# Performance work log

Measured on AMD Instinct MI355X. Metric: run time of the kernel, lower is better.

The kernel has to match this reference:

```python
import jax, jax.numpy as jnp
import numpy as np

B, NX, NR, D, H = 8, 512, 512, 256, 256


def setup_inputs() -> dict:
    key = jax.random.key(0)
    ks = jax.random.split(key, 8)
    s = 1.0 / np.sqrt(D)
    sh = 1.0 / np.sqrt(H)
    return {
        "X": jax.random.normal(ks[0], (B, NX, D), dtype=jnp.float32),
        "ref": jax.random.normal(ks[1], (B, NR, D), dtype=jnp.float32),
        "W_X": jax.random.normal(ks[2], (H, D), dtype=jnp.float32) * s,
        "b_X": jax.random.normal(ks[3], (H,), dtype=jnp.float32) * s,
        "W_ref": jax.random.normal(ks[4], (H, D), dtype=jnp.float32) * s,
        "b_ref": jax.random.normal(ks[5], (H,), dtype=jnp.float32) * s,
        "v_w": jax.random.normal(ks[6], (1, H), dtype=jnp.float32) * sh,
        "v_b": jax.random.normal(ks[7], (1,), dtype=jnp.float32) * sh,
    }


def reference(X, ref, W_X, b_X, W_ref, b_ref, v_w, v_b):
    # linear projections: [B, nX, H], [B, nR, H]
    hX = jnp.einsum('bxd,hd->bxh', X, W_X) + b_X
    hR = jnp.einsum('brd,hd->brh', ref, W_ref) + b_ref
    # additive (Bahdanau) scores: [B, nX, nR]
    t = jnp.tanh(hX[:, :, None, :] + hR[:, None, :, :])
    out = jnp.einsum('bxrh,h->bxr', t, v_w[0]) + v_b[0]
    # softmax over the n_X axis (dim=1 in torch)
    attn = jax.nn.softmax(out, axis=1)
    # weighted sum of X per ref position: [B, nR, D]
    weighted_X = jnp.einsum('bxe,bxr->bre', X, attn)
    return weighted_X
```

## Files before the change

kernel.cpp:

```cpp
#include <hip/hip_runtime.h>
#include <math.h>

#define CB 8
#define CNX 512
#define CNR 512
#define CD 256
#define CH 256

__device__ __forceinline__ float fast_rcp(float x) {
#if __has_builtin(__builtin_amdgcn_rcpf)
  return __builtin_amdgcn_rcpf(x);
#else
  return 1.0f / x;
#endif
}
__device__ __forceinline__ float fast_exp2(float x) {
#if __has_builtin(__builtin_amdgcn_exp2f)
  return __builtin_amdgcn_exp2f(x);
#else
  return exp2f(x);
#endif
}

__global__ __launch_bounds__(256) void proj_fused(
    const float* __restrict__ A0, const float* __restrict__ A1,
    const float* __restrict__ W0, const float* __restrict__ W1,
    const float* __restrict__ bias0, const float* __restrict__ bias1,
    float* __restrict__ E0, float* __restrict__ E1) {
  __shared__ float As[16][68];
  __shared__ float Ws[16][68];
  const int K = CD;
  int z = blockIdx.z;
  const float* A = z ? A1 : A0;
  const float* W = z ? W1 : W0;
  const float* bias = z ? bias1 : bias0;
  float* ET = z ? E1 : E0;
  int m0 = blockIdx.x * 64, n0 = blockIdx.y * 64;
  int tid = threadIdx.x;
  int tx = tid & 15, ty = tid >> 4;
  int lrow = tid >> 2, lc4 = tid & 3;
  int krot = (tid >> 6) << 2;
  float acc[4][4] = {};
  const float* pA = A + (size_t)(m0 + lrow) * K + lc4 * 4;
  const float* pW = W + (size_t)(n0 + lrow) * K + lc4 * 4;
  float4 av = *(const float4*)(pA);
  float4 wv = *(const float4*)(pW);
  for (int kt = 0; kt < K; kt += 16) {
    __syncthreads();
    As[lc4 * 4 + 0][lrow] = av.x;
    As[lc4 * 4 + 1][lrow] = av.y;
    As[lc4 * 4 + 2][lrow] = av.z;
    As[lc4 * 4 + 3][lrow] = av.w;
    Ws[lc4 * 4 + 0][lrow] = wv.x;
    Ws[lc4 * 4 + 1][lrow] = wv.y;
    Ws[lc4 * 4 + 2][lrow] = wv.z;
    Ws[lc4 * 4 + 3][lrow] = wv.w;
    __syncthreads();
    if (kt + 16 < K) {
      av = *(const float4*)(pA + kt + 16);
      wv = *(const float4*)(pW + kt + 16);
    }
#pragma unroll
    for (int k = 0; k < 16; k++) {
      int kk = (k + krot) & 15;
      float4 a4 = *(const float4*)&As[kk][ty * 4];
      float4 w4 = *(const float4*)&Ws[kk][tx * 4];
      float am[4] = {a4.x, a4.y, a4.z, a4.w};
      float wm[4] = {w4.x, w4.y, w4.z, w4.w};
#pragma unroll
      for (int i = 0; i < 4; i++)
#pragma unroll
        for (int j = 0; j < 4; j++)
          acc[i][j] = fmaf(am[i], wm[j], acc[i][j]);
    }
  }
  const float K2L = 2.8853900817779268f;
  float4 bv = *(const float4*)(bias + n0 + tx * 4);
  float bm[4] = {bv.x, bv.y, bv.z, bv.w};
  int b = m0 >> 9;
  int xbase = (m0 & 511) + ty * 4;
#pragma unroll
  for (int j = 0; j < 4; j++) {
    int h = n0 + tx * 4 + j;
    float4 o = {fast_exp2(K2L * (acc[0][j] + bm[j])),
                fast_exp2(K2L * (acc[1][j] + bm[j])),
                fast_exp2(K2L * (acc[2][j] + bm[j])),
                fast_exp2(K2L * (acc[3][j] + bm[j]))};
    *(float4*)(ET + ((size_t)b * CH + h) * CNX + xbase) = o;
  }
}

__global__ __launch_bounds__(512) void scores_kernel(
    const float* __restrict__ exT, const float* __restrict__ erT,
    const float* __restrict__ v_w, float* __restrict__ scT) {
  __shared__ float smem[4 * 2048 + 256];
  int b = blockIdx.z;
  int x0 = blockIdx.x * 64, r0 = blockIdx.y * 64;
  int tid = threadIdx.x;
  int g = tid >> 8;
  int t = tid & 255;
  float* xs = smem + g * 4096;
  float* rs = xs + 2048;
  float* vsh = smem + 8192;
  if (tid < 256) vsh[tid] = v_w[tid];
  int tx = t & 15, ty = t >> 4;
  int sr = t >> 4, sc = (t & 15) * 4;
  int wrot = (tid >> 6) & 7;
  const float* pX = exT + (size_t)b * CH * CNX + x0 + sc;
  const float* pR = erT + (size_t)b * CH * CNR + r0 + sc;
  int hb = g * 32;
  float4 xa0 = *(const float4*)(pX + (size_t)(hb + sr) * CNX);
  float4 xa1 = *(const float4*)(pX + (size_t)(hb + sr + 16) * CNX);
  float4 ra0 = *(const float4*)(pR + (size_t)(hb + sr) * CNR);
  float4 ra1 = *(const float4*)(pR + (size_t)(hb + sr + 16) * CNR);
  float acc[4][4] = {};
  for (int hc = hb; hc < CH; hc += 64) {
    __syncthreads();
    *(float4*)&xs[sr * 64 + sc] = xa0;
    *(float4*)&xs[(sr + 16) * 64 + sc] = xa1;
    *(float4*)&rs[sr * 64 + sc] = ra0;
    *(float4*)&rs[(sr + 16) * 64 + sc] = ra1;
    __syncthreads();
    if (hc + 64 < CH) {
      xa0 = *(const float4*)(pX + (size_t)(hc + 64 + sr) * CNX);
      xa1 = *(const float4*)(pX + (size_t)(hc + 64 + sr + 16) * CNX);
      ra0 = *(const float4*)(pR + (size_t)(hc + 64 + sr) * CNR);
      ra1 = *(const float4*)(pR + (size_t)(hc + 64 + sr + 16) * CNR);
    }
#pragma unroll 2
    for (int hq = 0; hq < 8; hq++) {
      int h0 = ((hq + wrot) & 7) * 4;
      float4 vv = *(const float4*)&vsh[hc + h0];
      float4 xv0 = *(const float4*)&xs[(h0 + 0) * 64 + tx * 4];
      float4 xv1 = *(const float4*)&xs[(h0 + 1) * 64 + tx * 4];
      float4 xv2 = *(const float4*)&xs[(h0 + 2) * 64 + tx * 4];
      float4 xv3 = *(const float4*)&xs[(h0 + 3) * 64 + tx * 4];
      float4 rv0 = *(const float4*)&rs[(h0 + 0) * 64 + ty * 4];
      float4 rv1 = *(const float4*)&rs[(h0 + 1) * 64 + ty * 4];
      float4 rv2 = *(const float4*)&rs[(h0 + 2) * 64 + ty * 4];
      float4 rv3 = *(const float4*)&rs[(h0 + 3) * 64 + ty * 4];
      float xm0[4] = {xv0.x, xv0.y, xv0.z, xv0.w};
      float xm1[4] = {xv1.x, xv1.y, xv1.z, xv1.w};
      float xm2[4] = {xv2.x, xv2.y, xv2.z, xv2.w};
      float xm3[4] = {xv3.x, xv3.y, xv3.z, xv3.w};
      float rm0[4] = {rv0.x, rv0.y, rv0.z, rv0.w};
      float rm1[4] = {rv1.x, rv1.y, rv1.z, rv1.w};
      float rm2[4] = {rv2.x, rv2.y, rv2.z, rv2.w};
      float rm3[4] = {rv3.x, rv3.y, rv3.z, rv3.w};
#pragma unroll
      for (int i = 0; i < 4; i++)
#pragma unroll
        for (int j = 0; j < 4; j++) {
          float a = fmaf(rm0[i], xm0[j], 1.0f);
          float bb = fmaf(rm1[i], xm1[j], 1.0f);
          float c = fmaf(rm2[i], xm2[j], 1.0f);
          float d = fmaf(rm3[i], xm3[j], 1.0f);
          float q12 = a * bb, q34 = c * d;
          float p12 = fmaf(vv.y, a, vv.x * bb);
          float p34 = fmaf(vv.w, c, vv.z * d);
          float num = fmaf(p34, q12, p12 * q34);
          acc[i][j] = fmaf(num, fast_rcp(q12 * q34), acc[i][j]);
        }
    }
  }
  __syncthreads();
  float* mg = smem;
  if (g == 1) {
#pragma unroll
    for (int i = 0; i < 4; i++)
#pragma unroll
      for (int j = 0; j < 4; j++)
        mg[t + 256 * (i * 4 + j)] = acc[i][j];
  }
  __syncthreads();
  if (g == 0) {
    float* pO = scT + ((size_t)b * CNR + r0 + ty * 4) * CNX + x0 + tx * 4;
#pragma unroll
    for (int i = 0; i < 4; i++) {
      float4 o = {-2.0f * (acc[i][0] + mg[t + 256 * (i * 4 + 0)]),
                  -2.0f * (acc[i][1] + mg[t + 256 * (i * 4 + 1)]),
                  -2.0f * (acc[i][2] + mg[t + 256 * (i * 4 + 2)]),
                  -2.0f * (acc[i][3] + mg[t + 256 * (i * 4 + 3)])};
      *(float4*)(pO + (size_t)i * CNX) = o;
    }
  }
}

__global__ __launch_bounds__(512) void wsum_fused(
    const float* __restrict__ scT, const float* __restrict__ X,
    float* __restrict__ out) {
  __shared__ float smem[4 * 2176 + 128];
  const float L2E = 1.4426950408889634f;
  int b = blockIdx.z;
  int r0 = blockIdx.x * 64, d0 = blockIdx.y * 64;
  int tid = threadIdx.x;
  int g = tid >> 8;
  int t = tid & 255;
  float* As = smem + g * 4352;
  float* Bs = As + 2176;
  float* dnn = smem + 8704;
  int tx = t & 15, ty = t >> 4;
  int ar = t >> 2, ak = (t & 3) * 4;
  int br = t >> 4, bc = (t & 15) * 4;
  int krot = ((tid >> 6) & 7) * 4;
  int kb = g * 32;
  const float* pS = scT + ((size_t)b * CNR + r0 + ar) * CNX + ak;
  const float* pB = X + (size_t)b * CNX * CD + d0 + bc;
  float acc[4][4] = {};
  float dsum = 0.0f;
  float4 s0 = *(const float4*)(pS + kb);
  float4 s1 = *(const float4*)(pS + kb + 16);
  float4 b0 = *(const float4*)(pB + (size_t)(kb + br) * CD);
  float4 b1 = *(const float4*)(pB + (size_t)(kb + br + 16) * CD);
  for (int kt = kb; kt < CNX; kt += 64) {
    float4 e0 = {fast_exp2(s0.x * L2E), fast_exp2(s0.y * L2E),
                 fast_exp2(s0.z * L2E), fast_exp2(s0.w * L2E)};
    float4 e1 = {fast_exp2(s1.x * L2E), fast_exp2(s1.y * L2E),
                 fast_exp2(s1.z * L2E), fast_exp2(s1.w * L2E)};
    dsum += ((e0.x + e0.y) + (e0.z + e0.w)) + ((e1.x + e1.y) + (e1.z + e1.w));
    __syncthreads();
    As[(ak + 0) * 68 + ar] = e0.x;
    As[(ak + 1) * 68 + ar] = e0.y;
    As[(ak + 2) * 68 + ar] = e0.z;
    As[(ak + 3) * 68 + ar] = e0.w;
    As[(ak + 16) * 68 + ar] = e1.x;
    As[(ak + 17) * 68 + ar] = e1.y;
    As[(ak + 18) * 68 + ar] = e1.z;
    As[(ak + 19) * 68 + ar] = e1.w;
    *(float4*)&Bs[br * 68 + bc] = b0;
    *(float4*)&Bs[(br + 16) * 68 + bc] = b1;
    __syncthreads();
    if (kt + 64 < CNX) {
      s0 = *(const float4*)(pS + kt + 64);
      s1 = *(const float4*)(pS + kt + 80);
      b0 = *(const float4*)(pB + (size_t)(kt + 64 + br) * CD);
      b1 = *(const float4*)(pB + (size_t)(kt + 64 + br + 16) * CD);
    }
#pragma unroll 8
    for (int k = 0; k < 32; k++) {
      int kk = (k + krot) & 31;
      float4 a4 = *(const float4*)&As[kk * 68 + ty * 4];
      float4 b4 = *(const float4*)&Bs[kk * 68 + tx * 4];
      float am[4] = {a4.x, a4.y, a4.z, a4.w};
      float bm[4] = {b4.x, b4.y, b4.z, b4.w};
#pragma unroll
      for (int i = 0; i < 4; i++)
#pragma unroll
        for (int j = 0; j < 4; j++)
          acc[i][j] = fmaf(am[i], bm[j], acc[i][j]);
    }
  }
  dsum += __shfl_xor(dsum, 1, 64);
  dsum += __shfl_xor(dsum, 2, 64);
  if ((t & 3) == 0) dnn[g * 64 + ar] = dsum;
  __syncthreads();
  float* mg = smem;
  if (g == 1) {
#pragma unroll
    for (int i = 0; i < 4; i++)
#pragma unroll
      for (int j = 0; j < 4; j++)
        mg[t + 256 * (i * 4 + j)] = acc[i][j];
  }
  __syncthreads();
  if (g == 0) {
    float invm[4];
#pragma unroll
    for (int i = 0; i < 4; i++)
      invm[i] = fast_rcp(dnn[ty * 4 + i] + dnn[64 + ty * 4 + i]);
    float* pO = out + ((size_t)b * CNR + r0 + ty * 4) * CD + d0 + tx * 4;
#pragma unroll
    for (int i = 0; i < 4; i++) {
      float4 o = {
          (acc[i][0] + mg[t + 256 * (i * 4 + 0)]) * invm[i],
          (acc[i][1] + mg[t + 256 * (i * 4 + 1)]) * invm[i],
          (acc[i][2] + mg[t + 256 * (i * 4 + 2)]) * invm[i],
          (acc[i][3] + mg[t + 256 * (i * 4 + 3)]) * invm[i]};
      *(float4*)(pO + (size_t)i * CD) = o;
    }
  }
}

extern "C" void kernel_launch(void* const* d_in, const int* in_sizes, int n_in,
                              void* d_out, int out_size, void* d_ws, size_t ws_size,
                              hipStream_t stream) {
  const float* X     = (const float*)d_in[0];
  const float* ref   = (const float*)d_in[1];
  const float* W_X   = (const float*)d_in[2];
  const float* b_X   = (const float*)d_in[3];
  const float* W_ref = (const float*)d_in[4];
  const float* b_ref = (const float*)d_in[5];
  const float* v_w   = (const float*)d_in[6];
  float* out = (float*)d_out;
  float* ws  = (float*)d_ws;

  float* exT = ws;
  float* erT = ws + 1048576;
  float* scT = ws + 2097152;

  proj_fused<<<dim3(64, 4, 2), 256, 0, stream>>>(X, ref, W_X, W_ref, b_X, b_ref, exT, erT);
  scores_kernel<<<dim3(8, 8, 8), 512, 0, stream>>>(exT, erT, v_w, scT);
  wsum_fused<<<dim3(8, 4, 8), 512, 0, stream>>>(scT, X, out);
}
```

Baseline: 152.8 us.

## Use split-bf16 MFMA for the projection GEMM instead of FP32 FMAs

Measured after the change: 146.3 us. -4.3%, faster.

```diff
diff --git a/kernel.cpp b/kernel.cpp
--- a/kernel.cpp
+++ b/kernel.cpp
@@ -6,6 +6,9 @@
 #define CNR 512
 #define CD 256
 #define CH 256
+
+typedef __attribute__((ext_vector_type(8))) short short8;
+typedef __attribute__((ext_vector_type(4))) float f32x4;
 
 __device__ __forceinline__ float fast_rcp(float x) {
 #if __has_builtin(__builtin_amdgcn_rcpf)
@@ -22,13 +25,41 @@
 #endif
 }
 
-__global__ __launch_bounds__(256) void proj_fused(
+__device__ __forceinline__ void cvt_store(unsigned short* dstH,
+                                          unsigned short* dstL,
+                                          float4 v0, float4 v1) {
+  unsigned u0x = __float_as_uint(v0.x), u0y = __float_as_uint(v0.y);
+  unsigned u0z = __float_as_uint(v0.z), u0w = __float_as_uint(v0.w);
+  unsigned u1x = __float_as_uint(v1.x), u1y = __float_as_uint(v1.y);
+  unsigned u1z = __float_as_uint(v1.z), u1w = __float_as_uint(v1.w);
+  uint4 H;
+  H.x = (u0x >> 16) | (u0y & 0xFFFF0000u);
+  H.y = (u0z >> 16) | (u0w & 0xFFFF0000u);
+  H.z = (u1x >> 16) | (u1y & 0xFFFF0000u);
+  H.w = (u1z >> 16) | (u1w & 0xFFFF0000u);
+  float r0x = v0.x - __uint_as_float(u0x & 0xFFFF0000u);
+  float r0y = v0.y - __uint_as_float(u0y & 0xFFFF0000u);
+  float r0z = v0.z - __uint_as_float(u0z & 0xFFFF0000u);
+  float r0w = v0.w - __uint_as_float(u0w & 0xFFFF0000u);
+  float r1x = v1.x - __uint_as_float(u1x & 0xFFFF0000u);
+  float r1y = v1.y - __uint_as_float(u1y & 0xFFFF0000u);
+  float r1z = v1.z - __uint_as_float(u1z & 0xFFFF0000u);
+  float r1w = v1.w - __uint_as_float(u1w & 0xFFFF0000u);
+  uint4 L;
+  L.x = (__float_as_uint(r0x) >> 16) | (__float_as_uint(r0y) & 0xFFFF0000u);
+  L.y = (__float_as_uint(r0z) >> 16) | (__float_as_uint(r0w) & 0xFFFF0000u);
+  L.z = (__float_as_uint(r1x) >> 16) | (__float_as_uint(r1y) & 0xFFFF0000u);
+  L.w = (__float_as_uint(r1z) >> 16) | (__float_as_uint(r1w) & 0xFFFF0000u);
+  *(uint4*)dstH = H;
+  *(uint4*)dstL = L;
+}
+
+__global__ __launch_bounds__(256) void proj_mfma(
     const float* __restrict__ A0, const float* __restrict__ A1,
     const float* __restrict__ W0, const float* __restrict__ W1,
     const float* __restrict__ bias0, const float* __restrict__ bias1,
     float* __restrict__ E0, float* __restrict__ E1) {
-  __shared__ float As[16][68];
-  __shared__ float Ws[16][68];
+  __shared__ unsigned short lds[2][4][64][40];
   const int K = CD;
   int z = blockIdx.z;
   const float* A = z ? A1 : A0;
@@ -37,56 +68,71 @@
   float* ET = z ? E1 : E0;
   int m0 = blockIdx.x * 64, n0 = blockIdx.y * 64;
   int tid = threadIdx.x;
-  int tx = tid & 15, ty = tid >> 4;
-  int lrow = tid >> 2, lc4 = tid & 3;
-  int krot = (tid >> 6) << 2;
-  float acc[4][4] = {};
-  const float* pA = A + (size_t)(m0 + lrow) * K + lc4 * 4;
-  const float* pW = W + (size_t)(n0 + lrow) * K + lc4 * 4;
-  float4 av = *(const float4*)(pA);
-  float4 wv = *(const float4*)(pW);
-  for (int kt = 0; kt < K; kt += 16) {
-    __syncthreads();
-    As[lc4 * 4 + 0][lrow] = av.x;
-    As[lc4 * 4 + 1][lrow] = av.y;
-    As[lc4 * 4 + 2][lrow] = av.z;
-    As[lc4 * 4 + 3][lrow] = av.w;
-    Ws[lc4 * 4 + 0][lrow] = wv.x;
-    Ws[lc4 * 4 + 1][lrow] = wv.y;
-    Ws[lc4 * 4 + 2][lrow] = wv.z;
-    Ws[lc4 * 4 + 3][lrow] = wv.w;
-    __syncthreads();
-    if (kt + 16 < K) {
-      av = *(const float4*)(pA + kt + 16);
-      wv = *(const float4*)(pW + kt + 16);
-    }
-#pragma unroll
-    for (int k = 0; k < 16; k++) {
-      int kk = (k + krot) & 15;
-      float4 a4 = *(const float4*)&As[kk][ty * 4];
-      float4 w4 = *(const float4*)&Ws[kk][tx * 4];
-      float am[4] = {a4.x, a4.y, a4.z, a4.w};
-      float wm[4] = {w4.x, w4.y, w4.z, w4.w};
-#pragma unroll
-      for (int i = 0; i < 4; i++)
-#pragma unroll
-        for (int j = 0; j < 4; j++)
-          acc[i][j] = fmaf(am[i], wm[j], acc[i][j]);
+  int lane = tid & 63, w = tid >> 6;
+  int wm = w >> 1, wn = w & 1;
+  int r = tid >> 2, kq = (tid & 3) * 8;
+  const float* pA = A + (size_t)(m0 + r) * K + kq;
+  const float* pW = W + (size_t)(n0 + r) * K + kq;
+  f32x4 acc[2][2] = {};
+  float4 a0 = *(const float4*)(pA);
+  float4 a1 = *(const float4*)(pA + 4);
+  float4 w0 = *(const float4*)(pW);
+  float4 w1 = *(const float4*)(pW + 4);
+  cvt_store(&lds[0][0][r][kq], &lds[0][1][r][kq], a0, a1);
+  cvt_store(&lds[0][2][r][kq], &lds[0][3][r][kq], w0, w1);
+  for (int s = 0; s < 8; s++) {
+    __syncthreads();
+    if (s < 7) {
+      int kt = (s + 1) * 32;
+      a0 = *(const float4*)(pA + kt);
+      a1 = *(const float4*)(pA + kt + 4);
+      w0 = *(const float4*)(pW + kt);
+      w1 = *(const float4*)(pW + kt + 4);
+    }
+    int cur = s & 1;
+    int arow = wm * 32 + (lane & 15);
+    int brow = wn * 32 + (lane & 15);
+    int koff = (lane >> 4) * 8;
+    short8 ah0 = *(const short8*)&lds[cur][0][arow][koff];
+    short8 ah1 = *(const short8*)&lds[cur][0][arow + 16][koff];
+    short8 al0 = *(const short8*)&lds[cur][1][arow][koff];
+    short8 al1 = *(const short8*)&lds[cur][1][arow + 16][koff];
+    short8 bh0 = *(const short8*)&lds[cur][2][brow][koff];
+    short8 bh1 = *(const short8*)&lds[cur][2][brow + 16][koff];
+    short8 bl0 = *(const short8*)&lds[cur][3][brow][koff];
+    short8 bl1 = *(const short8*)&lds[cur][3][brow + 16][koff];
+    acc[0][0] = __builtin_amdgcn_mfma_f32_16x16x32_bf16(ah0, bh0, acc[0][0], 0, 0, 0);
+    acc[0][1] = __builtin_amdgcn_mfma_f32_16x16x32_bf16(ah0, bh1, acc[0][1], 0, 0, 0);
+    acc[1][0] = __builtin_amdgcn_mfma_f32_16x16x32_bf16(ah1, bh0, acc[1][0], 0, 0, 0);
+    acc[1][1] = __builtin_amdgcn_mfma_f32_16x16x32_bf16(ah1, bh1, acc[1][1], 0, 0, 0);
+    acc[0][0] = __builtin_amdgcn_mfma_f32_16x16x32_bf16(ah0, bl0, acc[0][0], 0, 0, 0);
+    acc[0][1] = __builtin_amdgcn_mfma_f32_16x16x32_bf16(ah0, bl1, acc[0][1], 0, 0, 0);
+    acc[1][0] = __builtin_amdgcn_mfma_f32_16x16x32_bf16(ah1, bl0, acc[1][0], 0, 0, 0);
+    acc[1][1] = __builtin_amdgcn_mfma_f32_16x16x32_bf16(ah1, bl1, acc[1][1], 0, 0, 0);
+    acc[0][0] = __builtin_amdgcn_mfma_f32_16x16x32_bf16(al0, bh0, acc[0][0], 0, 0, 0);
+    acc[0][1] = __builtin_amdgcn_mfma_f32_16x16x32_bf16(al0, bh1, acc[0][1], 0, 0, 0);
+    acc[1][0] = __builtin_amdgcn_mfma_f32_16x16x32_bf16(al1, bh0, acc[1][0], 0, 0, 0);
+    acc[1][1] = __builtin_amdgcn_mfma_f32_16x16x32_bf16(al1, bh1, acc[1][1], 0, 0, 0);
+    if (s < 7) {
+      int nxt = cur ^ 1;
+      cvt_store(&lds[nxt][0][r][kq], &lds[nxt][1][r][kq], a0, a1);
+      cvt_store(&lds[nxt][2][r][kq], &lds[nxt][3][r][kq], w0, w1);
     }
   }
   const float K2L = 2.8853900817779268f;
-  float4 bv = *(const float4*)(bias + n0 + tx * 4);
-  float bm[4] = {bv.x, bv.y, bv.z, bv.w};
   int b = m0 >> 9;
-  int xbase = (m0 & 511) + ty * 4;
-#pragma unroll
-  for (int j = 0; j < 4; j++) {
-    int h = n0 + tx * 4 + j;
-    float4 o = {fast_exp2(K2L * (acc[0][j] + bm[j])),
-                fast_exp2(K2L * (acc[1][j] + bm[j])),
-                fast_exp2(K2L * (acc[2][j] + bm[j])),
-                fast_exp2(K2L * (acc[3][j] + bm[j]))};
-    *(float4*)(ET + ((size_t)b * CH + h) * CNX + xbase) = o;
+  int xq = (m0 & 511) + wm * 32 + (lane >> 4) * 4;
+#pragma unroll
+  for (int mi = 0; mi < 2; mi++) {
+#pragma unroll
+    for (int ni = 0; ni < 2; ni++) {
+      int h = n0 + wn * 32 + ni * 16 + (lane & 15);
+      float bb = bias[h];
+      f32x4 a = acc[mi][ni];
+      float4 o = {fast_exp2(K2L * (a[0] + bb)), fast_exp2(K2L * (a[1] + bb)),
+                  fast_exp2(K2L * (a[2] + bb)), fast_exp2(K2L * (a[3] + bb))};
+      *(float4*)(ET + ((size_t)b * CH + h) * CNX + xq + mi * 16) = o;
+    }
   }
 }
 
@@ -298,7 +344,7 @@
   float* erT = ws + 1048576;
   float* scT = ws + 2097152;
 
-  proj_fused<<<dim3(64, 4, 2), 256, 0, stream>>>(X, ref, W_X, W_ref, b_X, b_ref, exT, erT);
+  proj_mfma<<<dim3(64, 4, 2), 256, 0, stream>>>(X, ref, W_X, W_ref, b_X, b_ref, exT, erT);
   scores_kernel<<<dim3(8, 8, 8), 512, 0, stream>>>(exT, erT, v_w, scT);
   wsum_fused<<<dim3(8, 4, 8), 512, 0, stream>>>(scT, X, out);
 }
```
